# Kernel tuning notes

Measured on AMD Instinct MI355X. Metric: run time of the kernel, lower is better.

Reference implementation:

```python
import jax, jax.numpy as jnp
from jax import lax
import numpy as np

B, N_PER = 4, 8192          # equal-sized point clouds
RATIO, K = 0.5, 16
C_IN, C_OUT = 64, 128
M_PER = int(N_PER * RATIO)  # FPS samples per cloud
BN_EPS = 1e-5


def setup_inputs() -> dict:
    key = jax.random.key(0)
    k1, k2, k3 = jax.random.split(key, 3)
    N = B * N_PER
    x = jax.random.normal(k1, (N, C_IN), jnp.float32)
    pos = jax.random.uniform(k2, (N, 3), jnp.float32)
    batch = jnp.repeat(jnp.arange(B, dtype=jnp.int32), N_PER)
    W = jax.random.normal(k3, (C_IN, C_OUT), jnp.float32) / np.sqrt(C_IN).astype(np.float32)
    b = jnp.zeros((C_OUT,), jnp.float32)
    gamma = jnp.ones((C_OUT,), jnp.float32)
    beta = jnp.zeros((C_OUT,), jnp.float32)
    return {"x": x, "pos": pos, "batch": batch, "W": W, "b": b, "gamma": gamma, "beta": beta}


def _fps_single(pos_b):
    # Deterministic farthest point sampling on one cloud [N_PER, 3] -> [M_PER] indices.
    n = pos_b.shape[0]
    def step(carry, _):
        dists, last = carry
        d = jnp.sum((pos_b - pos_b[last]) ** 2, axis=-1)
        dists = jnp.minimum(dists, d)
        nxt = jnp.argmax(dists).astype(jnp.int32)
        return (dists, nxt), nxt
    init = (jnp.full((n,), jnp.inf, pos_b.dtype), jnp.int32(0))
    _, idx = lax.scan(step, init, None, length=M_PER - 1)
    return jnp.concatenate([jnp.zeros((1,), jnp.int32), idx])


def reference(x, pos, batch, W, b, gamma, beta):
    # batch is assumed to be B contiguous equal segments of N_PER points.
    pos_b = pos.reshape(B, N_PER, 3)
    samp = jax.vmap(_fps_single)(pos_b)                                # [B, M_PER]
    new_pos = jnp.take_along_axis(pos_b, samp[:, :, None], axis=1)     # [B, M_PER, 3]

    # kNN of each sampled point among all points of the same cloud (squared L2).
    sq_p = jnp.sum(pos_b * pos_b, axis=-1)                              # [B, N_PER]
    sq_q = jnp.sum(new_pos * new_pos, axis=-1)                          # [B, M_PER]
    d2 = sq_q[:, :, None] + sq_p[:, None, :] - 2.0 * jnp.einsum('bmd,bnd->bmn', new_pos, pos_b)
    _, nbr = lax.top_k(-d2, K)                                          # [B, M_PER, K]

    # MLP: Linear -> BatchNorm1d (batch stats over all N points) -> exact GELU.
    h = x @ W + b                                                       # [N, C_OUT]
    mean = jnp.mean(h, axis=0)
    var = jnp.var(h, axis=0)
    h = (h - mean) / jnp.sqrt(var + BN_EPS) * gamma + beta
    h = jax.nn.gelu(h, approximate=False)

    h_b = h.reshape(B, N_PER, C_OUT)
    gathered = jax.vmap(lambda hb, nb: hb[nb])(h_b, nbr)                # [B, M_PER, K, C_OUT]
    new_x = jnp.max(gathered, axis=2)                                   # scatter-max == max over k neighbors

    new_batch = jnp.repeat(jnp.arange(B, dtype=batch.dtype), M_PER)
    return new_x.reshape(B * M_PER, C_OUT), new_pos.reshape(B * M_PER, 3), new_batch
```

## Files before the change

### kernel.cpp

```cpp
#include <hip/hip_runtime.h>
#include <math.h>

#define NB    4
#define NPER  8192
#define MPER  4096
#define NTOT  32768
#define MTOT  16384
#define COUT  128
#define NWORK 252

#define NEWPOS_OFF 2097152
#define NEWB_OFF   2146304

#define WS_H     0u
#define WS_SQP   16777216u
#define WS_SAMP  16908288u
#define WS_PART  16973824u
#define WS_PART2 17006592u
#define WS_STAT  17039360u

__global__ void misc_kernel(const float* __restrict__ pos, float* __restrict__ sqp,
                            float* __restrict__ out) {
  int g = blockIdx.x * 1024 + threadIdx.x;
  if (g < NTOT) {
    float x = pos[g * 3 + 0], y = pos[g * 3 + 1], z = pos[g * 3 + 2];
    sqp[g] = fmaf(z, z, fmaf(x, x, __fmul_rn(y, y)));
  }
  if (g < MTOT) out[NEWB_OFF + g] = (float)(g >> 12);
}

__global__ __launch_bounds__(256) void matmul_kernel(const float* __restrict__ x,
                                                     const float* __restrict__ W,
                                                     const float* __restrict__ bias,
                                                     float* __restrict__ h) {
  __shared__ float xs[16][64];
  const int tid = threadIdx.x;
  const int rowbase = blockIdx.x * 16;
  for (int i = tid; i < 16 * 64; i += 256) xs[i >> 6][i & 63] = x[rowbase * 64 + i];
  __syncthreads();
  const int col = tid & 127;
  const int rs = (tid >> 7) * 8;
  float acc[8] = {0.f, 0.f, 0.f, 0.f, 0.f, 0.f, 0.f, 0.f};
  for (int k = 0; k < 64; ++k) {
    float wv = W[k * 128 + col];
#pragma unroll
    for (int r = 0; r < 8; ++r) acc[r] = fmaf(xs[rs + r][k], wv, acc[r]);
  }
  float bb = bias[col];
#pragma unroll
  for (int r = 0; r < 8; ++r) h[(rowbase + rs + r) * 128 + col] = acc[r] + bb;
}

__global__ __launch_bounds__(256) void stats_kernel(const float* __restrict__ h,
                                                    float* __restrict__ part,
                                                    float* __restrict__ part2) {
  const int tid = threadIdx.x;
  const int col = tid & 127;
  const int half = tid >> 7;
  const int r0 = blockIdx.x * 512;
  float s = 0.f, s2 = 0.f;
  for (int r = r0 + half; r < r0 + 512; r += 2) {
    float v = h[r * 128 + col];
    s += v;
    s2 = fmaf(v, v, s2);
  }
  __shared__ float ps[2][128], ps2[2][128];
  ps[half][col] = s;
  ps2[half][col] = s2;
  __syncthreads();
  if (half == 0) {
    part[blockIdx.x * 128 + col] = ps[0][col] + ps[1][col];
    part2[blockIdx.x * 128 + col] = ps2[0][col] + ps2[1][col];
  }
}

__global__ void finalize_kernel(const float* __restrict__ part,
                                const float* __restrict__ part2,
                                float* __restrict__ stat) {
  int col = threadIdx.x;
  float s = 0.f, s2 = 0.f;
  for (int i = 0; i < 64; ++i) {
    s += part[i * 128 + col];
    s2 += part2[i * 128 + col];
  }
  float mean = s / 32768.0f;
  float var = s2 / 32768.0f - mean * mean;
  float invstd = 1.0f / sqrtf(var + 1e-5f);
  stat[col] = mean;
  stat[128 + col] = invstd;
}

__global__ __launch_bounds__(256) void bngelu_kernel(float* __restrict__ h,
                                                     const float* __restrict__ stat,
                                                     const float* __restrict__ gamma,
                                                     const float* __restrict__ beta) {
  int base = blockIdx.x * 2048 + threadIdx.x;
#pragma unroll
  for (int t = 0; t < 8; ++t) {
    int g = base + t * 256;
    int col = g & 127;
    float v = h[g];
    float z = (v - stat[col]) * stat[128 + col];
    z = z * gamma[col] + beta[col];
    float ge = 0.5f * z * (1.0f + erff(z * 0.70710678118654752440f));
    h[g] = ge;
  }
}

#define UMAXU(a, b) (((a) > (b)) ? (a) : (b))
#define UMINU(a, b) (((a) < (b)) ? (a) : (b))
#define DPP_FMAX(m, CTRL)                                                       \
  {                                                                             \
    int t_ = __builtin_amdgcn_update_dpp(__float_as_int(m), __float_as_int(m),  \
                                         (CTRL), 0xf, 0xf, false);              \
    m = fmaxf(m, __int_as_float(t_));                                           \
  }
#define DPP_UMIN(c, CTRL)                                                       \
  {                                                                             \
    unsigned int t_ = (unsigned int)__builtin_amdgcn_update_dpp(                \
        (int)(c), (int)(c), (CTRL), 0xf, 0xf, false);                           \
    c = UMINU(c, t_);                                                           \
  }
#define DPP_KMIN64(lo, hi, CTRL)                                                \
  {                                                                             \
    unsigned int a_ = (unsigned int)__builtin_amdgcn_update_dpp(                \
        (int)(lo), (int)(lo), (CTRL), 0xf, 0xf, false);                         \
    unsigned int b_ = (unsigned int)__builtin_amdgcn_update_dpp(                \
        (int)(hi), (int)(hi), (CTRL), 0xf, 0xf, false);                         \
    unsigned long long nk_ = ((unsigned long long)b_ << 32) | a_;               \
    unsigned long long ok_ = ((unsigned long long)(hi) << 32) | (lo);           \
    bool t_ = nk_ < ok_;                                                        \
    lo = t_ ? a_ : (lo); hi = t_ ? b_ : (hi);                                   \
  }
#define FPS_DECL(i) float px##i, py##i, pz##i, dd##i;
#define FPS_LOAD(i)                     \
  {                                     \
    const int n = tid + (i) * 512;      \
    px##i = p[n * 3 + 0];               \
    py##i = p[n * 3 + 1];               \
    pz##i = p[n * 3 + 2];               \
    dd##i = INFINITY;                   \
    lpxy[n] = make_float2(px##i, py##i);\
    lpz[n] = pz##i;                     \
  }
#define FPS_PIN(i) \
  asm volatile("" : "+v"(px##i), "+v"(py##i), "+v"(pz##i));
#define FPS_DIST(i)                                                             \
  {                                                                             \
    float dx = __fsub_rn(px##i, lx), dy = __fsub_rn(py##i, ly),                 \
          dz = __fsub_rn(pz##i, lz);                                            \
    float d = fmaf(dz, dz, fmaf(dx, dx, __fmul_rn(dy, dy)));                    \
    float nd = fminf(dd##i, d);                                                 \
    dd##i = nd;                                                                 \
    m = fmaxf(m, nd);                                                           \
  }
#define FPS_MATCH(i)                                                            \
  ci = (dd##i == D) ? (unsigned int)(tid + (i) * 512) : ci;

__global__ __launch_bounds__(512)
__attribute__((amdgpu_waves_per_eu(2, 2)))
void fused_kernel(const float* __restrict__ pos, const float* __restrict__ sqp,
                  const float* __restrict__ h, int* __restrict__ samp,
                  float* __restrict__ out) {
  __shared__ __align__(16) unsigned char smem[98816];
  const int tid = threadIdx.x;
  const int wv = tid >> 6;
  if (blockIdx.x < NB) {
    const int b = blockIdx.x;
    const float* p = pos + b * NPER * 3;
    float2* lpxy = (float2*)smem;
    float* lpz = (float*)(smem + 65536);
    unsigned int* slotD = (unsigned int*)(smem + 98304);
    unsigned int* slotI = (unsigned int*)(smem + 98336);
    FPS_DECL(0) FPS_DECL(1) FPS_DECL(2) FPS_DECL(3)
    FPS_DECL(4) FPS_DECL(5) FPS_DECL(6) FPS_DECL(7)
    FPS_DECL(8) FPS_DECL(9) FPS_DECL(10) FPS_DECL(11)
    FPS_DECL(12) FPS_DECL(13) FPS_DECL(14) FPS_DECL(15)
    FPS_LOAD(0) FPS_LOAD(1) FPS_LOAD(2) FPS_LOAD(3)
    FPS_LOAD(4) FPS_LOAD(5) FPS_LOAD(6) FPS_LOAD(7)
    FPS_LOAD(8) FPS_LOAD(9) FPS_LOAD(10) FPS_LOAD(11)
    FPS_LOAD(12) FPS_LOAD(13) FPS_LOAD(14) FPS_LOAD(15)
    FPS_PIN(0) FPS_PIN(1) FPS_PIN(2) FPS_PIN(3)
    FPS_PIN(4) FPS_PIN(5) FPS_PIN(6) FPS_PIN(7)
    FPS_PIN(8) FPS_PIN(9) FPS_PIN(10) FPS_PIN(11)
    FPS_PIN(12) FPS_PIN(13) FPS_PIN(14) FPS_PIN(15)
    float lx = p[0], ly = p[1], lz = p[2];
    if (tid == 0) {
      __hip_atomic_store(&samp[b * MPER], 0, __ATOMIC_RELAXED,
                         __HIP_MEMORY_SCOPE_AGENT);
      out[NEWPOS_OFF + (b * MPER) * 3 + 0] = lx;
      out[NEWPOS_OFF + (b * MPER) * 3 + 1] = ly;
      out[NEWPOS_OFF + (b * MPER) * 3 + 2] = lz;
    }
    __syncthreads();
    for (int s = 1; s < MPER; ++s) {
      float m = 0.0f;
      FPS_DIST(0) FPS_DIST(1) FPS_DIST(2) FPS_DIST(3)
      FPS_DIST(4) FPS_DIST(5) FPS_DIST(6) FPS_DIST(7)
      FPS_DIST(8) FPS_DIST(9) FPS_DIST(10) FPS_DIST(11)
      FPS_DIST(12) FPS_DIST(13) FPS_DIST(14) FPS_DIST(15)
      DPP_FMAX(m, 0x111)
      DPP_FMAX(m, 0x112)
      DPP_FMAX(m, 0x114)
      DPP_FMAX(m, 0x118)
      DPP_FMAX(m, 0x142)
      DPP_FMAX(m, 0x143)
      if ((tid & 63) == 63) slotD[wv] = __float_as_uint(m);
      __syncthreads();
      const uint4* spD = (const uint4*)slotD;
      uint4 a0 = spD[0], a1 = spD[1];
      unsigned int r0 = UMAXU(UMAXU(a0.x, a0.y), UMAXU(a0.z, a0.w));
      unsigned int r1 = UMAXU(UMAXU(a1.x, a1.y), UMAXU(a1.z, a1.w));
      const float D = __uint_as_float(UMAXU(r0, r1));
      unsigned int ci = 0xFFFFFFFFu;
      FPS_MATCH(15) FPS_MATCH(14) FPS_MATCH(13) FPS_MATCH(12)
      FPS_MATCH(11) FPS_MATCH(10) FPS_MATCH(9) FPS_MATCH(8)
      FPS_MATCH(7) FPS_MATCH(6) FPS_MATCH(5) FPS_MATCH(4)
      FPS_MATCH(3) FPS_MATCH(2) FPS_MATCH(1) FPS_MATCH(0)
      DPP_UMIN(ci, 0x111)
      DPP_UMIN(ci, 0x112)
      DPP_UMIN(ci, 0x114)
      DPP_UMIN(ci, 0x118)
      DPP_UMIN(ci, 0x142)
      DPP_UMIN(ci, 0x143)
      if ((tid & 63) == 63) slotI[wv] = ci;
      __syncthreads();
      const uint4* spI = (const uint4*)slotI;
      uint4 b0 = spI[0], b1 = spI[1];
      unsigned int i0 = UMINU(UMINU(b0.x, b0.y), UMINU(b0.z, b0.w));
      unsigned int i1 = UMINU(UMINU(b1.x, b1.y), UMINU(b1.z, b1.w));
      const int widx = (int)UMINU(i0, i1);
      float2 wxy = lpxy[widx];
      float wz = lpz[widx];
      lx = wxy.x; ly = wxy.y; lz = wz;
      if (tid == 0) {
        __hip_atomic_store(&samp[b * MPER + s], widx, __ATOMIC_RELAXED,
                           __HIP_MEMORY_SCOPE_AGENT);
        out[NEWPOS_OFF + (b * MPER + s) * 3 + 0] = lx;
        out[NEWPOS_OFF + (b * MPER + s) * 3 + 1] = ly;
        out[NEWPOS_OFF + (b * MPER + s) * 3 + 2] = lz;
      }
    }
  } else {
    float* dist = (float*)smem;
    unsigned long long* ckey = (unsigned long long*)(smem + 32768);
    int* sidx_sh = (int*)(smem + 32768 + 128);
    const int w = (int)blockIdx.x - NB;
    for (int j = w; j < MTOT; j += NWORK) {
      const int b = j & 3;
      const int s = j >> 2;
      const int q = (b << 12) | s;
      if (tid == 0) {
        int v;
        for (;;) {
          v = __hip_atomic_load(&samp[q], __ATOMIC_RELAXED,
                                __HIP_MEMORY_SCOPE_AGENT);
          if ((unsigned int)v < (unsigned int)NPER) break;
          __builtin_amdgcn_s_sleep(64);
        }
        sidx_sh[0] = v;
      }
      __syncthreads();
      const int sidx = sidx_sh[0];
      const int gbase = b * NPER;
      const float qx = pos[(gbase + sidx) * 3 + 0];
      const float qy = pos[(gbase + sidx) * 3 + 1];
      const float qz = pos[(gbase + sidx) * 3 + 2];
      const float sqq = sqp[gbase + sidx];
      unsigned long long lkey = ~0ull;
      for (int i = 0; i < 16; ++i) {
        int n = tid + i * 512;
        int g = gbase + n;
        float dot = fmaf(qz, pos[g * 3 + 2],
                         fmaf(qy, pos[g * 3 + 1], __fmul_rn(qx, pos[g * 3 + 0])));
        float d2 = __fsub_rn(__fadd_rn(sqq, sqp[g]), __fmul_rn(2.0f, dot));
        dist[n] = d2;
        unsigned int ub = __float_as_uint(d2);
        ub = (ub & 0x80000000u) ? ~ub : (ub | 0x80000000u);
        unsigned long long key = ((unsigned long long)ub << 32) | (unsigned int)n;
        lkey = (key < lkey) ? key : lkey;
      }
      __syncthreads();
      float mx = -INFINITY;
      for (int r = 0; r < 16; ++r) {
        const int pr = r & 1;
        unsigned int klo = (unsigned int)lkey;
        unsigned int khi = (unsigned int)(lkey >> 32);
        DPP_KMIN64(klo, khi, 0x111)
        DPP_KMIN64(klo, khi, 0x112)
        DPP_KMIN64(klo, khi, 0x114)
        DPP_KMIN64(klo, khi, 0x118)
        DPP_KMIN64(klo, khi, 0x142)
        DPP_KMIN64(klo, khi, 0x143)
        if ((tid & 63) == 63)
          ckey[pr * 8 + wv] = ((unsigned long long)khi << 32) | klo;
        __syncthreads();
        const ulonglong2* cp = (const ulonglong2*)(ckey + pr * 8);
        ulonglong2 c0 = cp[0], c1 = cp[1], c2 = cp[2], c3 = cp[3];
        unsigned long long k0 = (c0.x < c0.y) ? c0.x : c0.y;
        unsigned long long k1 = (c1.x < c1.y) ? c1.x : c1.y;
        unsigned long long k2 = (c2.x < c2.y) ? c2.x : c2.y;
        unsigned long long k3 = (c3.x < c3.y) ? c3.x : c3.y;
        k0 = (k1 < k0) ? k1 : k0;
        k2 = (k3 < k2) ? k3 : k2;
        k0 = (k2 < k0) ? k2 : k0;
        const int n = (int)(unsigned int)(k0 & 0xFFFFFFFFull);
        if (tid < COUT) mx = fmaxf(mx, h[(gbase + n) * 128 + tid]);
        if (tid == (n & 511)) {
          dist[n] = INFINITY;
          lkey = ~0ull;
          for (int i = 0; i < 16; ++i) {
            int nn = tid + i * 512;
            unsigned int ub = __float_as_uint(dist[nn]);
            ub = (ub & 0x80000000u) ? ~ub : (ub | 0x80000000u);
            unsigned long long kk =
                ((unsigned long long)ub << 32) | (unsigned int)nn;
            lkey = (kk < lkey) ? kk : lkey;
          }
        }
      }
      __syncthreads();
      if (tid < COUT) out[q * 128 + tid] = mx;
    }
  }
}

extern "C" void kernel_launch(void* const* d_in, const int* in_sizes, int n_in,
                              void* d_out, int out_size, void* d_ws, size_t ws_size,
                              hipStream_t stream) {
  (void)in_sizes; (void)n_in; (void)out_size; (void)ws_size;
  const float* x     = (const float*)d_in[0];
  const float* pos   = (const float*)d_in[1];
  const float* W     = (const float*)d_in[3];
  const float* bias  = (const float*)d_in[4];
  const float* gamma = (const float*)d_in[5];
  const float* beta  = (const float*)d_in[6];
  float* out = (float*)d_out;
  char* ws = (char*)d_ws;
  float* h     = (float*)(ws + WS_H);
  float* sqp   = (float*)(ws + WS_SQP);
  int*   samp  = (int*)(ws + WS_SAMP);
  float* part  = (float*)(ws + WS_PART);
  float* part2 = (float*)(ws + WS_PART2);
  float* stat  = (float*)(ws + WS_STAT);

  misc_kernel<<<dim3(32), dim3(1024), 0, stream>>>(pos, sqp, out);
  matmul_kernel<<<dim3(2048), dim3(256), 0, stream>>>(x, W, bias, h);
  stats_kernel<<<dim3(64), dim3(256), 0, stream>>>(h, part, part2);
  finalize_kernel<<<dim3(1), dim3(128), 0, stream>>>(part, part2, stat);
  bngelu_kernel<<<dim3(2048), dim3(256), 0, stream>>>(h, stat, gamma, beta);
  fused_kernel<<<dim3(256), dim3(512), 0, stream>>>(pos, sqp, h, samp, out);
}
```

Measured before the change: 3.362 ms.

## Fuse BN+GELU into kNN gather and compute squared norms inline

Removes the separate misc and BN+GELU kernels. BatchNorm plus exact GELU is now applied on the fly to each gathered neighbor feature inside the kNN max loop, and point squared norms are recomputed from pos instead of being read from a precomputed buffer. The new_batch output is written by the worker blocks. This saves two launches and a full read-modify-write pass over h, at the cost of recomputing erf for every gathered element (K per output, roughly 2x the elementwise work) inside the latency-bound worker loop.

```diff
diff --git a/kernel.cpp b/kernel.cpp
--- a/kernel.cpp
+++ b/kernel.cpp
@@ -13,21 +13,10 @@
 #define NEWB_OFF   2146304
 
 #define WS_H     0u
-#define WS_SQP   16777216u
 #define WS_SAMP  16908288u
 #define WS_PART  16973824u
 #define WS_PART2 17006592u
 #define WS_STAT  17039360u
-
-__global__ void misc_kernel(const float* __restrict__ pos, float* __restrict__ sqp,
-                            float* __restrict__ out) {
-  int g = blockIdx.x * 1024 + threadIdx.x;
-  if (g < NTOT) {
-    float x = pos[g * 3 + 0], y = pos[g * 3 + 1], z = pos[g * 3 + 2];
-    sqp[g] = fmaf(z, z, fmaf(x, x, __fmul_rn(y, y)));
-  }
-  if (g < MTOT) out[NEWB_OFF + g] = (float)(g >> 12);
-}
 
 __global__ __launch_bounds__(256) void matmul_kernel(const float* __restrict__ x,
                                                      const float* __restrict__ W,
@@ -90,23 +79,6 @@
   stat[128 + col] = invstd;
 }
 
-__global__ __launch_bounds__(256) void bngelu_kernel(float* __restrict__ h,
-                                                     const float* __restrict__ stat,
-                                                     const float* __restrict__ gamma,
-                                                     const float* __restrict__ beta) {
-  int base = blockIdx.x * 2048 + threadIdx.x;
-#pragma unroll
-  for (int t = 0; t < 8; ++t) {
-    int g = base + t * 256;
-    int col = g & 127;
-    float v = h[g];
-    float z = (v - stat[col]) * stat[128 + col];
-    z = z * gamma[col] + beta[col];
-    float ge = 0.5f * z * (1.0f + erff(z * 0.70710678118654752440f));
-    h[g] = ge;
-  }
-}
-
 #define UMAXU(a, b) (((a) > (b)) ? (a) : (b))
 #define UMINU(a, b) (((a) < (b)) ? (a) : (b))
 #define DPP_FMAX(m, CTRL)                                                       \
@@ -159,8 +131,9 @@
 
 __global__ __launch_bounds__(512)
 __attribute__((amdgpu_waves_per_eu(2, 2)))
-void fused_kernel(const float* __restrict__ pos, const float* __restrict__ sqp,
-                  const float* __restrict__ h, int* __restrict__ samp,
+void fused_kernel(const float* __restrict__ pos, const float* __restrict__ h,
+                  int* __restrict__ samp, const float* __restrict__ stat,
+                  const float* __restrict__ gamma, const float* __restrict__ beta,
                   float* __restrict__ out) {
   __shared__ __align__(16) unsigned char smem[98816];
   const int tid = threadIdx.x;
@@ -246,6 +219,17 @@
     unsigned long long* ckey = (unsigned long long*)(smem + 32768);
     int* sidx_sh = (int*)(smem + 32768 + 128);
     const int w = (int)blockIdx.x - NB;
+    {
+      int g = w * 512 + tid;
+      if (g < MTOT) out[NEWB_OFF + g] = (float)(g >> 12);
+    }
+    float bn_mean = 0.f, bn_istd = 0.f, bn_g = 0.f, bn_b = 0.f;
+    if (tid < COUT) {
+      bn_mean = stat[tid];
+      bn_istd = stat[128 + tid];
+      bn_g = gamma[tid];
+      bn_b = beta[tid];
+    }
     for (int j = w; j < MTOT; j += NWORK) {
       const int b = j & 3;
       const int s = j >> 2;
@@ -266,14 +250,15 @@
       const float qx = pos[(gbase + sidx) * 3 + 0];
       const float qy = pos[(gbase + sidx) * 3 + 1];
       const float qz = pos[(gbase + sidx) * 3 + 2];
-      const float sqq = sqp[gbase + sidx];
+      const float sqq = fmaf(qz, qz, fmaf(qx, qx, __fmul_rn(qy, qy)));
       unsigned long long lkey = ~0ull;
       for (int i = 0; i < 16; ++i) {
         int n = tid + i * 512;
         int g = gbase + n;
-        float dot = fmaf(qz, pos[g * 3 + 2],
-                         fmaf(qy, pos[g * 3 + 1], __fmul_rn(qx, pos[g * 3 + 0])));
-        float d2 = __fsub_rn(__fadd_rn(sqq, sqp[g]), __fmul_rn(2.0f, dot));
+        float xg = pos[g * 3 + 0], yg = pos[g * 3 + 1], zg = pos[g * 3 + 2];
+        float dot = fmaf(qz, zg, fmaf(qy, yg, __fmul_rn(qx, xg)));
+        float sqg = fmaf(zg, zg, fmaf(xg, xg, __fmul_rn(yg, yg)));
+        float d2 = __fsub_rn(__fadd_rn(sqq, sqg), __fmul_rn(2.0f, dot));
         dist[n] = d2;
         unsigned int ub = __float_as_uint(d2);
         ub = (ub & 0x80000000u) ? ~ub : (ub | 0x80000000u);
@@ -305,7 +290,13 @@
         k2 = (k3 < k2) ? k3 : k2;
         k0 = (k2 < k0) ? k2 : k0;
         const int n = (int)(unsigned int)(k0 & 0xFFFFFFFFull);
-        if (tid < COUT) mx = fmaxf(mx, h[(gbase + n) * 128 + tid]);
+        if (tid < COUT) {
+          float v = h[(gbase + n) * 128 + tid];
+          float z = (v - bn_mean) * bn_istd;
+          z = z * bn_g + bn_b;
+          float ge = 0.5f * z * (1.0f + erff(z * 0.70710678118654752440f));
+          mx = fmaxf(mx, ge);
+        }
         if (tid == (n & 511)) {
           dist[n] = INFINITY;
           lkey = ~0ull;
@@ -338,16 +329,14 @@
   float* out = (float*)d_out;
   char* ws = (char*)d_ws;
   float* h     = (float*)(ws + WS_H);
-  float* sqp   = (float*)(ws + WS_SQP);
   int*   samp  = (int*)(ws + WS_SAMP);
   float* part  = (float*)(ws + WS_PART);
   float* part2 = (float*)(ws + WS_PART2);
   float* stat  = (float*)(ws + WS_STAT);
 
-  misc_kernel<<<dim3(32), dim3(1024), 0, stream>>>(pos, sqp, out);
   matmul_kernel<<<dim3(2048), dim3(256), 0, stream>>>(x, W, bias, h);
   stats_kernel<<<dim3(64), dim3(256), 0, stream>>>(h, part, part2);
   finalize_kernel<<<dim3(1), dim3(128), 0, stream>>>(part, part2, stat);
-  bngelu_kernel<<<dim3(2048), dim3(256), 0, stream>>>(h, stat, gamma, beta);
-  fused_kernel<<<dim3(256), dim3(512), 0, stream>>>(pos, sqp, h, samp, out);
-}
+  fused_kernel<<<dim3(256), dim3(512), 0, stream>>>(pos, h, samp, stat, gamma,
+                                                    beta, out);
+}
```

New measurement: 3.334 ms. No clear change (-0.8%).
